# Kernel tuning notes

Measured on AMD Instinct MI355X. Metric: run time of the kernel, lower is better.

Reference implementation:

```python
import jax, jax.numpy as jnp
import numpy as np

NEG_SLOPE = 0.2  # PyG GATConv default negative_slope


def _gat_layer(x, src, dst, n_nodes, W, a_src, a_dst, b):
    # x: [N, din]; src/dst: [E] (self-loops already included)
    h = x @ W                                  # [N, dout]
    s_src = h @ a_src                          # [N]
    s_dst = h @ a_dst                          # [N]
    e = jax.nn.leaky_relu(s_src[src] + s_dst[dst], NEG_SLOPE)  # [E]
    # per-target-node softmax over incoming edges (stable via segment max)
    m = jax.ops.segment_max(e, dst, num_segments=n_nodes)      # [N]
    a = jnp.exp(e - m[dst])                    # [E]
    denom = jax.ops.segment_sum(a, dst, num_segments=n_nodes)  # [N]
    msg = h[src] * a[:, None]                  # [E, dout]
    agg = jax.ops.segment_sum(msg, dst, num_segments=n_nodes)  # [N, dout]
    return agg / denom[:, None] + b


def setup_inputs() -> dict:
    key = jax.random.key(0)
    ks = jax.random.split(key, 16)
    N, E = 100000, 1600000
    in_dim, hid_dim, out_dim = 128, 128, 64
    x = jax.random.normal(ks[0], (N, in_dim), dtype=jnp.float32)
    edge_idx = jax.random.randint(ks[1], (2, E), 0, N, dtype=jnp.int32)

    def lin(k, din, dout):
        return jax.random.normal(k, (din, dout), dtype=jnp.float32) * (1.0 / np.sqrt(din))

    def att(k, dout):
        return jax.random.normal(k, (dout,), dtype=jnp.float32) * (1.0 / np.sqrt(dout))

    return {
        "x": x, "edge_idx": edge_idx,
        "W1": lin(ks[2], in_dim, hid_dim), "as1": att(ks[3], hid_dim), "ad1": att(ks[4], hid_dim), "b1": jnp.zeros((hid_dim,), jnp.float32),
        "W2": lin(ks[5], hid_dim, hid_dim), "as2": att(ks[6], hid_dim), "ad2": att(ks[7], hid_dim), "b2": jnp.zeros((hid_dim,), jnp.float32),
        "W3": lin(ks[8], hid_dim, out_dim), "as3": att(ks[9], out_dim), "ad3": att(ks[10], out_dim), "b3": jnp.zeros((out_dim,), jnp.float32),
    }


def reference(x, edge_idx, W1, as1, ad1, b1, W2, as2, ad2, b2, W3, as3, ad3, b3):
    N = x.shape[0]
    # add self-loops (PyG GATConv default add_self_loops=True)
    loops = jnp.arange(N, dtype=edge_idx.dtype)
    src = jnp.concatenate([edge_idx[0], loops])
    dst = jnp.concatenate([edge_idx[1], loops])
    h = _gat_layer(x, src, dst, N, W1, as1, ad1, b1)
    h = _gat_layer(h, src, dst, N, W2, as2, ad2, b2)
    h = _gat_layer(h, src, dst, N, W3, as3, ad3, b3)
    return jnp.mean(h, axis=-2)  # [out_dim]
```

## Files before the change

### kernel.cpp

```cpp
#include <hip/hip_runtime.h>

static inline int ceil_div(long long a, long long b) { return (int)((a + b - 1) / b); }

typedef __attribute__((ext_vector_type(8))) short bf16x8;
typedef __attribute__((ext_vector_type(4))) float f32x4;

#define TILE 8192
#define BKSH 9

__device__ __forceinline__ float lrelu(float t) { return t > 0.f ? t : 0.2f * t; }

__device__ __forceinline__ void atomAddF(float* p, float v) {
  unsafeAtomicAdd(p, v);
}

__device__ __forceinline__ unsigned int f2bf(float f) {
  unsigned int u = __float_as_uint(f);
  unsigned int r = ((u >> 16) & 1u) + 0x7fffu;
  return (u + r) >> 16;
}

__global__ void cvt_bf16(const float* __restrict__ X, unsigned short* __restrict__ Xb, int n4) {
  int i = blockIdx.x * blockDim.x + threadIdx.x;
  if (i < n4) {
    const float4 v = ((const float4*)X)[i];
    uint2 o;
    o.x = f2bf(v.x) | (f2bf(v.y) << 16);
    o.y = f2bf(v.z) | (f2bf(v.w) << 16);
    ((uint2*)Xb)[i] = o;
  }
}

__global__ void transpose_all(const float* __restrict__ W1, const float* __restrict__ W2,
                              const float* __restrict__ W3, unsigned short* __restrict__ Wt1,
                              unsigned short* __restrict__ Wt2, unsigned short* __restrict__ Wt3) {
  int idx = blockIdx.x * blockDim.x + threadIdx.x;
  const float* W; unsigned short* Wt; int local, DOUTv;
  if (idx < 16384)      { W = W1; Wt = Wt1; local = idx;          DOUTv = 128; }
  else if (idx < 32768) { W = W2; Wt = Wt2; local = idx - 16384;  DOUTv = 128; }
  else if (idx < 40960) { W = W3; Wt = Wt3; local = idx - 32768;  DOUTv = 64;  }
  else return;
  const int k = local / DOUTv, n = local % DOUTv;
  Wt[n * 128 + k] = (unsigned short)f2bf(W[local]);
}

template<int DOUT>
__launch_bounds__(256)
__global__ void gemm_mfma(const unsigned short* __restrict__ Xb, const unsigned short* __restrict__ Wt,
                          const float* __restrict__ avs, const float* __restrict__ avd,
                          unsigned short* __restrict__ Hb, float* __restrict__ Ss,
                          float* __restrict__ Sd, int N, int RG) {
  constexpr int DIN = 128;
  constexpr int CG = DOUT / 64;
  constexpr int RPB = 4 / CG;
  __shared__ float sps[RPB][2][64], spd[RPB][2][64];

  const int wv = threadIdx.x >> 6;
  const int rgl = wv / CG;
  const int cg  = wv % CG;
  const int rg = blockIdx.x * RPB + rgl;
  const bool active = rg < RG;
  const int lane = threadIdx.x & 63;
  const int l16 = lane & 15, quad = lane >> 4;
  const int row0 = rg * 64, colw0 = cg * 64;

  if (active) {
    int xoff[4], woff[4];
#pragma unroll
    for (int t = 0; t < 4; t++) {
      int m = row0 + t * 16 + l16; if (m > N - 1) m = N - 1;
      xoff[t] = m * DIN + quad * 8;
      woff[t] = (colw0 + t * 16 + l16) * DIN + quad * 8;
    }

    f32x4 acc[4][4];
#pragma unroll
    for (int a = 0; a < 4; a++)
#pragma unroll
      for (int c = 0; c < 4; c++) acc[a][c] = (f32x4)0.f;

#pragma unroll
    for (int kk = 0; kk < 4; kk++) {
      bf16x8 aw[4], bx[4];
#pragma unroll
      for (int t = 0; t < 4; t++) aw[t] = *(const bf16x8*)(Wt + woff[t] + kk * 32);
#pragma unroll
      for (int t = 0; t < 4; t++) bx[t] = *(const bf16x8*)(Xb + xoff[t] + kk * 32);
#pragma unroll
      for (int wt = 0; wt < 4; wt++)
#pragma unroll
        for (int xt = 0; xt < 4; xt++)
          acc[wt][xt] = __builtin_amdgcn_mfma_f32_16x16x32_bf16(aw[wt], bx[xt], acc[wt][xt], 0, 0, 0);
    }

    float4 af[4], df[4];
#pragma unroll
    for (int wt = 0; wt < 4; wt++) {
      af[wt] = *(const float4*)(avs + colw0 + wt * 16 + quad * 4);
      df[wt] = *(const float4*)(avd + colw0 + wt * 16 + quad * 4);
    }
#pragma unroll
    for (int xt = 0; xt < 4; xt++) {
      const int m = row0 + xt * 16 + l16;
      float ps = 0.f, pd = 0.f;
#pragma unroll
      for (int wt = 0; wt < 4; wt++) {
        const f32x4 c = acc[wt][xt];
        ps += c[0]*af[wt].x + c[1]*af[wt].y + c[2]*af[wt].z + c[3]*af[wt].w;
        pd += c[0]*df[wt].x + c[1]*df[wt].y + c[2]*df[wt].z + c[3]*df[wt].w;
      }
      ps += __shfl_xor(ps, 16); ps += __shfl_xor(ps, 32);
      pd += __shfl_xor(pd, 16); pd += __shfl_xor(pd, 32);
      if (quad == 0) {
        if (CG == 2) {
          sps[rgl][cg][xt * 16 + l16] = ps;
          spd[rgl][cg][xt * 16 + l16] = pd;
        } else if (m < N) {
          Ss[m] = ps; Sd[m] = pd;
        }
      }
      if (m < N) {
        unsigned short* hp = Hb + (size_t)m * DOUT + colw0 + quad * 4;
#pragma unroll
        for (int wt = 0; wt < 4; wt++) {
          const f32x4 c = acc[wt][xt];
          uint2 o;
          o.x = f2bf(c[0]) | (f2bf(c[1]) << 16);
          o.y = f2bf(c[2]) | (f2bf(c[3]) << 16);
          *(uint2*)(hp + wt * 16) = o;
        }
      }
    }
  }
  if (CG == 2) {
    __syncthreads();
    if (active && cg == 0) {
      const int m = row0 + lane;
      if (m < N) {
        Ss[m] = sps[rgl][0][lane] + sps[rgl][1][lane];
        Sd[m] = spd[rgl][0][lane] + spd[rgl][1][lane];
      }
    }
  }
}

__launch_bounds__(256)
__global__ void bucket_hist(const int* __restrict__ dstv, int* __restrict__ bh,
                            int E, int NBUK) {
  __shared__ int h[256];
  h[threadIdx.x] = 0;
  __syncthreads();
  const int base = blockIdx.x * TILE;
  const int end = min(E, base + TILE);
  for (int i = base + threadIdx.x; i < end; i += 256)
    atomicAdd(&h[dstv[i] >> BKSH], 1);
  __syncthreads();
  if (threadIdx.x < NBUK) bh[blockIdx.x * NBUK + threadIdx.x] = h[threadIdx.x];
}

__launch_bounds__(256)
__global__ void col_scan(int* __restrict__ bh, int* __restrict__ tot, int NBA, int NBUK) {
  __shared__ int sc[256];
  const int t = threadIdx.x;
  const int b = blockIdx.x;
  int carry = 0;
  for (int c0 = 0; c0 < NBA; c0 += 256) {
    const int idx = c0 + t;
    const int v = (idx < NBA) ? bh[idx * NBUK + b] : 0;
    sc[t] = v;
    __syncthreads();
    for (int off = 1; off < 256; off <<= 1) {
      int u = (t >= off) ? sc[t - off] : 0;
      __syncthreads();
      sc[t] += u;
      __syncthreads();
    }
    if (idx < NBA) bh[idx * NBUK + b] = carry + sc[t] - v;
    carry += sc[255];
    __syncthreads();
  }
  if (t == 0) tot[b] = carry;
}

__launch_bounds__(256)
__global__ void base_scan(const int* __restrict__ tot, int* __restrict__ bucketBase,
                          int* __restrict__ rowptr_N, int NBUK, int E) {
  __shared__ int sc[256];
  const int t = threadIdx.x;
  int carry = 0;
  for (int c0 = 0; c0 < NBUK; c0 += 256) {
    const int idx = c0 + t;
    const int v = (idx < NBUK) ? tot[idx] : 0;
    sc[t] = v;
    __syncthreads();
    for (int off = 1; off < 256; off <<= 1) {
      int u = (t >= off) ? sc[t - off] : 0;
      __syncthreads();
      sc[t] += u;
      __syncthreads();
    }
    if (idx < NBUK) bucketBase[idx] = carry + sc[t] - v;
    carry += sc[255];
    __syncthreads();
  }
  if (t == 0) { bucketBase[NBUK] = E; *rowptr_N = E; }
}

__launch_bounds__(256)
__global__ void bucket_scatter(const int* __restrict__ src, const int* __restrict__ dstv,
                               const int* __restrict__ bh, const int* __restrict__ bucketBase,
                               unsigned int* __restrict__ pairs, int E, int NBUK) {
  __shared__ int ofs[256];
  if (threadIdx.x < NBUK)
    ofs[threadIdx.x] = bh[blockIdx.x * NBUK + threadIdx.x] + bucketBase[threadIdx.x];
  __syncthreads();
  const int base = blockIdx.x * TILE;
  const int end = min(E, base + TILE);
  for (int i = base + threadIdx.x; i < end; i += 256) {
    const int d = dstv[i];
    const int pos = atomicAdd(&ofs[d >> BKSH], 1);
    pairs[pos] = ((unsigned int)src[i] << BKSH) | (unsigned int)(d & ((1 << BKSH) - 1));
  }
}

__launch_bounds__(256)
__global__ void region_build(const unsigned int* __restrict__ pairs,
                             const int* __restrict__ bucketBase,
                             int* __restrict__ rowptr, int* __restrict__ srcs, int N) {
  __shared__ int cnt[512], ofs[512], ps[256];
  const int t = threadIdx.x;
  const int r = blockIdx.x;
  const int p0 = bucketBase[r], p1 = bucketBase[r + 1];
  cnt[t] = 0; cnt[t + 256] = 0;
  __syncthreads();
  for (int i = p0 + t; i < p1; i += 256)
    atomicAdd(&cnt[pairs[i] & 511u], 1);
  __syncthreads();
  const int c0 = cnt[2 * t], c1 = cnt[2 * t + 1];
  const int pr = c0 + c1;
  ps[t] = pr;
  __syncthreads();
  for (int off = 1; off < 256; off <<= 1) {
    int v = (t >= off) ? ps[t - off] : 0;
    __syncthreads();
    ps[t] += v;
    __syncthreads();
  }
  const int pbase = ps[t] - pr;
  ofs[2 * t] = pbase; ofs[2 * t + 1] = pbase + c0;
  __syncthreads();
  {
    const int d0 = (r << BKSH) + t;
    if (d0 < N) rowptr[d0] = p0 + ofs[t];
    const int d1 = (r << BKSH) + t + 256;
    if (d1 < N) rowptr[d1] = p0 + ofs[t + 256];
  }
  __syncthreads();
  for (int i = p0 + t; i < p1; i += 256) {
    const unsigned int w = pairs[i];
    const int pos = atomicAdd(&ofs[w & 511u], 1);
    srcs[p0 + pos] = (int)(w >> BKSH);
  }
}

template<int DOUT, bool OBF>
__launch_bounds__(256)
__global__ void node_gather(const int* __restrict__ rowptr, const int* __restrict__ srcs,
                            const float* __restrict__ Ss, const float* __restrict__ Sd,
                            const unsigned short* __restrict__ Hb, const float* __restrict__ b,
                            float* __restrict__ out, unsigned short* __restrict__ outb, int N) {
  constexpr int EPL = DOUT / 16;
  __shared__ uint2 swL[16][18];

  const int l16 = threadIdx.x & 15;
  const int grp = threadIdx.x >> 4;
  const int node = blockIdx.x * 16 + grp;
  if (node >= N) return;

  const int r0 = rowptr[node], r1 = rowptr[node + 1];
  const int deg = r1 - r0;
  const float sd = Sd[node];
  const float wself = __expf(lrelu(Ss[node] + sd));

  float acc[EPL];
#pragma unroll
  for (int k = 0; k < EPL; k++) acc[k] = 0.f;
  float lsum = 0.f;
  const size_t colb = (size_t)l16 * EPL;

  for (int j0 = 0; j0 < deg; j0 += 16) {
    const int idx = j0 + l16;
    int s = node; float w = 0.f;
    if (idx < deg) {
      s = srcs[r0 + idx];
      w = __expf(lrelu(Ss[s] + sd));
    }
    lsum += w;
    swL[grp][l16] = make_uint2((unsigned)s, __float_as_uint(w));
    const int cnt = min(16, deg - j0);
    int t = 0;
    for (; t + 4 <= cnt; t += 4) {
      const uint2 sw0 = swL[grp][t],     sw1 = swL[grp][t + 1];
      const uint2 sw2 = swL[grp][t + 2], sw3 = swL[grp][t + 3];
      const float w0 = __uint_as_float(sw0.y), w1 = __uint_as_float(sw1.y);
      const float w2 = __uint_as_float(sw2.y), w3 = __uint_as_float(sw3.y);
      if (EPL == 8) {
        const uint4 u0 = *(const uint4*)(Hb + (size_t)sw0.x * DOUT + colb);
        const uint4 u1 = *(const uint4*)(Hb + (size_t)sw1.x * DOUT + colb);
        const uint4 u2 = *(const uint4*)(Hb + (size_t)sw2.x * DOUT + colb);
        const uint4 u3 = *(const uint4*)(Hb + (size_t)sw3.x * DOUT + colb);
        const unsigned int a0[4] = {u0.x,u0.y,u0.z,u0.w}, a1[4] = {u1.x,u1.y,u1.z,u1.w};
        const unsigned int a2[4] = {u2.x,u2.y,u2.z,u2.w}, a3[4] = {u3.x,u3.y,u3.z,u3.w};
#pragma unroll
        for (int k = 0; k < 4; k++) {
          acc[2*k]   += __uint_as_float(a0[k] << 16) * w0 + __uint_as_float(a1[k] << 16) * w1
                      + __uint_as_float(a2[k] << 16) * w2 + __uint_as_float(a3[k] << 16) * w3;
          acc[2*k+1] += __uint_as_float(a0[k] & 0xffff0000u) * w0 + __uint_as_float(a1[k] & 0xffff0000u) * w1
                      + __uint_as_float(a2[k] & 0xffff0000u) * w2 + __uint_as_float(a3[k] & 0xffff0000u) * w3;
        }
      } else {
        const uint2 u0 = *(const uint2*)(Hb + (size_t)sw0.x * DOUT + colb);
        const uint2 u1 = *(const uint2*)(Hb + (size_t)sw1.x * DOUT + colb);
        const uint2 u2 = *(const uint2*)(Hb + (size_t)sw2.x * DOUT + colb);
        const uint2 u3 = *(const uint2*)(Hb + (size_t)sw3.x * DOUT + colb);
        const unsigned int a0[2] = {u0.x,u0.y}, a1[2] = {u1.x,u1.y};
        const unsigned int a2[2] = {u2.x,u2.y}, a3[2] = {u3.x,u3.y};
#pragma unroll
        for (int k = 0; k < 2; k++) {
          acc[2*k]   += __uint_as_float(a0[k] << 16) * w0 + __uint_as_float(a1[k] << 16) * w1
                      + __uint_as_float(a2[k] << 16) * w2 + __uint_as_float(a3[k] << 16) * w3;
          acc[2*k+1] += __uint_as_float(a0[k] & 0xffff0000u) * w0 + __uint_as_float(a1[k] & 0xffff0000u) * w1
                      + __uint_as_float(a2[k] & 0xffff0000u) * w2 + __uint_as_float(a3[k] & 0xffff0000u) * w3;
        }
      }
    }
    for (; t < cnt; t++) {
      const uint2 sw = swL[grp][t];
      const float w0 = __uint_as_float(sw.y);
      const unsigned short* pp = Hb + (size_t)sw.x * DOUT + colb;
#pragma unroll
      for (int k = 0; k < EPL / 2; k++) {
        const unsigned int u = ((const unsigned int*)pp)[k];
        acc[2*k]   += __uint_as_float(u << 16) * w0;
        acc[2*k+1] += __uint_as_float(u & 0xffff0000u) * w0;
      }
    }
  }

#pragma unroll
  for (int off = 8; off; off >>= 1) lsum += __shfl_xor(lsum, off);

  {
    const unsigned short* pp = Hb + (size_t)node * DOUT + colb;
#pragma unroll
    for (int k = 0; k < EPL / 2; k++) {
      const unsigned int u = ((const unsigned int*)pp)[k];
      acc[2*k]   += __uint_as_float(u << 16) * wself;
      acc[2*k+1] += __uint_as_float(u & 0xffff0000u) * wself;
    }
  }
  const float inv = 1.f / (lsum + wself);

  float o[EPL];
#pragma unroll
  for (int k = 0; k < EPL; k++) o[k] = acc[k] * inv + b[colb + k];
  if (OBF) {
    if (EPL == 8) {
      uint4 u;
      u.x = f2bf(o[0]) | (f2bf(o[1]) << 16);
      u.y = f2bf(o[2]) | (f2bf(o[3]) << 16);
      u.z = f2bf(o[4]) | (f2bf(o[5]) << 16);
      u.w = f2bf(o[6]) | (f2bf(o[7]) << 16);
      *(uint4*)(outb + (size_t)node * DOUT + colb) = u;
    } else {
      uint2 u;
      u.x = f2bf(o[0]) | (f2bf(o[1]) << 16);
      u.y = f2bf(o[2]) | (f2bf(o[3]) << 16);
      *(uint2*)(outb + (size_t)node * DOUT + colb) = u;
    }
  } else {
    float* op = out + (size_t)node * DOUT + colb;
#pragma unroll
    for (int k = 0; k < EPL; k += 4)
      *(float4*)(op + k) = make_float4(o[k], o[k+1], o[k+2], o[k+3]);
  }
}

__global__ void mean64(const float* __restrict__ Hf, float* __restrict__ out, int N, float scale) {
  __shared__ float sm[256];
  const int col = threadIdx.x & 63;
  const int seg = threadIdx.x >> 6;
  const int stride = gridDim.x * 4;
  float s = 0.f;
  for (int n = blockIdx.x * 4 + seg; n < N; n += stride) s += Hf[(size_t)n * 64 + col];
  sm[threadIdx.x] = s;
  __syncthreads();
  if (seg == 0) {
    float tot = sm[col] + sm[64 + col] + sm[128 + col] + sm[192 + col];
    atomAddF(&out[col], tot * scale);
  }
}

extern "C" void kernel_launch(void* const* d_in, const int* in_sizes, int n_in,
                              void* d_out, int out_size, void* d_ws, size_t ws_size,
                              hipStream_t stream) {
  const float* x   = (const float*)d_in[0];
  const int*   ei  = (const int*)d_in[1];
  const float* W1  = (const float*)d_in[2];
  const float* as1 = (const float*)d_in[3];
  const float* ad1 = (const float*)d_in[4];
  const float* b1  = (const float*)d_in[5];
  const float* W2  = (const float*)d_in[6];
  const float* as2 = (const float*)d_in[7];
  const float* ad2 = (const float*)d_in[8];
  const float* b2  = (const float*)d_in[9];
  const float* W3  = (const float*)d_in[10];
  const float* as3 = (const float*)d_in[11];
  const float* ad3 = (const float*)d_in[12];
  const float* b3  = (const float*)d_in[13];

  const int N = in_sizes[0] / 128;
  const int E = in_sizes[1] / 2;
  const int* src  = ei;
  const int* dstv = ei + E;
  const int RG = ceil_div(N, 64);
  const int NBA = ceil_div(E, TILE);
  const int NBUK = ceil_div(N, 1 << BKSH);

  float* p = (float*)d_ws;
  float* bufA = p; p += (size_t)N * 64;
  float* SsSd = p; p += (size_t)2 * N;
  float* Ss = SsSd, *Sd = SsSd + N;
  unsigned short* Xb = (unsigned short*)p; p += (size_t)N * 64;
  unsigned short* Hb = (unsigned short*)p; p += (size_t)N * 64;
  unsigned short* Wt1 = (unsigned short*)p; p += 128 * 128 / 2;
  unsigned short* Wt2 = (unsigned short*)p; p += 128 * 128 / 2;
  unsigned short* Wt3 = (unsigned short*)p; p += 128 * 64 / 2;
  int* ip = (int*)p;
  int* rowptr     = ip; ip += N + 1;
  int* bh         = ip; ip += (size_t)NBA * NBUK;
  int* tot        = ip; ip += NBUK;
  int* bucketBase = ip; ip += NBUK + 1;
  unsigned int* pairs = (unsigned int*)ip; ip += E;
  int* srcs       = ip; ip += E;

  bucket_hist<<<NBA, 256, 0, stream>>>(dstv, bh, E, NBUK);
  col_scan<<<NBUK, 256, 0, stream>>>(bh, tot, NBA, NBUK);
  base_scan<<<1, 256, 0, stream>>>(tot, bucketBase, rowptr + N, NBUK, E);
  bucket_scatter<<<NBA, 256, 0, stream>>>(src, dstv, bh, bucketBase, pairs, E, NBUK);
  region_build<<<NBUK, 256, 0, stream>>>(pairs, bucketBase, rowptr, srcs, N);

  transpose_all<<<ceil_div(40960, 256), 256, 0, stream>>>(W1, W2, W3, Wt1, Wt2, Wt3);
  cvt_bf16<<<ceil_div((long long)N * 32, 256), 256, 0, stream>>>(x, Xb, N * 32);

  const int GG = ceil_div(N, 16);
  gemm_mfma<128><<<ceil_div(RG, 2), 256, 0, stream>>>(Xb, Wt1, as1, ad1, Hb, Ss, Sd, N, RG);
  node_gather<128, true><<<GG, 256, 0, stream>>>(rowptr, srcs, Ss, Sd, Hb, b1, nullptr, Xb, N);
  gemm_mfma<128><<<ceil_div(RG, 2), 256, 0, stream>>>(Xb, Wt2, as2, ad2, Hb, Ss, Sd, N, RG);
  node_gather<128, true><<<GG, 256, 0, stream>>>(rowptr, srcs, Ss, Sd, Hb, b2, nullptr, Xb, N);
  gemm_mfma<64><<<ceil_div(RG, 4), 256, 0, stream>>>(Xb, Wt3, as3, ad3, Hb, Ss, Sd, N, RG);
  node_gather<64, false><<<GG, 256, 0, stream>>>(rowptr, srcs, Ss, Sd, Hb, b3, bufA, nullptr, N);

  hipMemsetAsync(d_out, 0, 64 * sizeof(float), stream);
  mean64<<<256, 256, 0, stream>>>(bufA, (float*)d_out, N, 1.0f / (float)N);
}
```

Before: 437.7 us.

## Fuse CSR build into cooperative kernel, merge prep kernels, fold mean into gather

The five CSR-construction kernels are merged into one cooperative kernel that separates its phases with grid-wide syncs. The bf16 conversion of x and the weight transposes now run in a single launch. The final layer's gather accumulates the column mean directly through shared and global atomics, which removes the fp32 intermediate buffer and the separate mean kernel. This cuts launch count and an N×64 write/read, at the cost of a CSR build capped at 256 blocks and many global atomics on the 64 outputs.

```diff
diff --git a/kernel.cpp b/kernel.cpp
--- a/kernel.cpp
+++ b/kernel.cpp
@@ -1,4 +1,5 @@
 #include <hip/hip_runtime.h>
+#include <hip/hip_cooperative_groups.h>
 
 static inline int ceil_div(long long a, long long b) { return (int)((a + b - 1) / b); }
 
@@ -20,7 +21,10 @@
   return (u + r) >> 16;
 }
 
-__global__ void cvt_bf16(const float* __restrict__ X, unsigned short* __restrict__ Xb, int n4) {
+__global__ void prep_all(const float* __restrict__ X, unsigned short* __restrict__ Xb, int n4,
+                         const float* __restrict__ W1, const float* __restrict__ W2,
+                         const float* __restrict__ W3, unsigned short* __restrict__ Wt1,
+                         unsigned short* __restrict__ Wt2, unsigned short* __restrict__ Wt3) {
   int i = blockIdx.x * blockDim.x + threadIdx.x;
   if (i < n4) {
     const float4 v = ((const float4*)X)[i];
@@ -28,20 +32,16 @@
     o.x = f2bf(v.x) | (f2bf(v.y) << 16);
     o.y = f2bf(v.z) | (f2bf(v.w) << 16);
     ((uint2*)Xb)[i] = o;
-  }
-}
-
-__global__ void transpose_all(const float* __restrict__ W1, const float* __restrict__ W2,
-                              const float* __restrict__ W3, unsigned short* __restrict__ Wt1,
-                              unsigned short* __restrict__ Wt2, unsigned short* __restrict__ Wt3) {
-  int idx = blockIdx.x * blockDim.x + threadIdx.x;
-  const float* W; unsigned short* Wt; int local, DOUTv;
-  if (idx < 16384)      { W = W1; Wt = Wt1; local = idx;          DOUTv = 128; }
-  else if (idx < 32768) { W = W2; Wt = Wt2; local = idx - 16384;  DOUTv = 128; }
-  else if (idx < 40960) { W = W3; Wt = Wt3; local = idx - 32768;  DOUTv = 64;  }
+    return;
+  }
+  int idx = i - n4;
+  const float* W; unsigned short* Wt; int DOUTv;
+  if (idx < 16384)      { W = W1; Wt = Wt1;               DOUTv = 128; }
+  else if (idx < 32768) { W = W2; Wt = Wt2; idx -= 16384; DOUTv = 128; }
+  else if (idx < 40960) { W = W3; Wt = Wt3; idx -= 32768; DOUTv = 64;  }
   else return;
-  const int k = local / DOUTv, n = local % DOUTv;
-  Wt[n * 128 + k] = (unsigned short)f2bf(W[local]);
+  const int k = idx / DOUTv, n = idx % DOUTv;
+  Wt[n * 128 + k] = (unsigned short)f2bf(W[idx]);
 }
 
 template<int DOUT>
@@ -145,259 +145,237 @@
 }
 
 __launch_bounds__(256)
-__global__ void bucket_hist(const int* __restrict__ dstv, int* __restrict__ bh,
-                            int E, int NBUK) {
-  __shared__ int h[256];
-  h[threadIdx.x] = 0;
-  __syncthreads();
-  const int base = blockIdx.x * TILE;
-  const int end = min(E, base + TILE);
-  for (int i = base + threadIdx.x; i < end; i += 256)
-    atomicAdd(&h[dstv[i] >> BKSH], 1);
-  __syncthreads();
-  if (threadIdx.x < NBUK) bh[blockIdx.x * NBUK + threadIdx.x] = h[threadIdx.x];
-}
-
-__launch_bounds__(256)
-__global__ void col_scan(int* __restrict__ bh, int* __restrict__ tot, int NBA, int NBUK) {
-  __shared__ int sc[256];
+__global__ void coop_csr(const int* __restrict__ src, const int* __restrict__ dstv,
+                         int* __restrict__ bh, int* __restrict__ tot,
+                         int* __restrict__ bucketBase, int* __restrict__ rowptr,
+                         unsigned int* __restrict__ pairs, int* __restrict__ srcs,
+                         int E, int N, int NBA, int NBUK) {
+  namespace cg = cooperative_groups;
+  cg::grid_group grid = cg::this_grid();
+  __shared__ int A[512], Bf[512], Cf[256];
   const int t = threadIdx.x;
-  const int b = blockIdx.x;
-  int carry = 0;
-  for (int c0 = 0; c0 < NBA; c0 += 256) {
-    const int idx = c0 + t;
-    const int v = (idx < NBA) ? bh[idx * NBUK + b] : 0;
-    sc[t] = v;
-    __syncthreads();
+
+  for (int blk = blockIdx.x; blk < NBA; blk += gridDim.x) {
+    A[t] = 0; __syncthreads();
+    const int base = blk * TILE, end = min(E, base + TILE);
+    for (int i = base + t; i < end; i += 256) atomicAdd(&A[dstv[i] >> BKSH], 1);
+    __syncthreads();
+    if (t < NBUK) bh[blk * NBUK + t] = A[t];
+    __syncthreads();
+  }
+  grid.sync();
+
+  for (int b = blockIdx.x; b < NBUK; b += gridDim.x) {
+    int carry = 0;
+    for (int c0 = 0; c0 < NBA; c0 += 256) {
+      const int idx = c0 + t;
+      const int v = (idx < NBA) ? bh[idx * NBUK + b] : 0;
+      A[t] = v; __syncthreads();
+      for (int off = 1; off < 256; off <<= 1) {
+        int u = (t >= off) ? A[t - off] : 0; __syncthreads();
+        A[t] += u; __syncthreads();
+      }
+      if (idx < NBA) bh[idx * NBUK + b] = carry + A[t] - v;
+      carry += A[255]; __syncthreads();
+    }
+    if (t == 0) tot[b] = carry;
+    __syncthreads();
+  }
+  grid.sync();
+
+  if (blockIdx.x == 0) {
+    int carry = 0;
+    for (int c0 = 0; c0 < NBUK; c0 += 256) {
+      const int idx = c0 + t;
+      const int v = (idx < NBUK) ? tot[idx] : 0;
+      A[t] = v; __syncthreads();
+      for (int off = 1; off < 256; off <<= 1) {
+        int u = (t >= off) ? A[t - off] : 0; __syncthreads();
+        A[t] += u; __syncthreads();
+      }
+      if (idx < NBUK) bucketBase[idx] = carry + A[t] - v;
+      carry += A[255]; __syncthreads();
+    }
+    if (t == 0) { bucketBase[NBUK] = E; rowptr[N] = E; }
+  }
+  grid.sync();
+
+  for (int blk = blockIdx.x; blk < NBA; blk += gridDim.x) {
+    if (t < NBUK) A[t] = bh[blk * NBUK + t] + bucketBase[t];
+    __syncthreads();
+    const int base = blk * TILE, end = min(E, base + TILE);
+    for (int i = base + t; i < end; i += 256) {
+      const int d = dstv[i];
+      const int pos = atomicAdd(&A[d >> BKSH], 1);
+      pairs[pos] = ((unsigned int)src[i] << BKSH) | (unsigned int)(d & ((1 << BKSH) - 1));
+    }
+    __syncthreads();
+  }
+  grid.sync();
+
+  for (int r = blockIdx.x; r < NBUK; r += gridDim.x) {
+    const int p0 = bucketBase[r], p1 = bucketBase[r + 1];
+    A[t] = 0; A[t + 256] = 0; __syncthreads();
+    for (int i = p0 + t; i < p1; i += 256) atomicAdd(&A[pairs[i] & 511u], 1);
+    __syncthreads();
+    const int c0 = A[2 * t], c1 = A[2 * t + 1];
+    const int pr = c0 + c1;
+    Cf[t] = pr; __syncthreads();
     for (int off = 1; off < 256; off <<= 1) {
-      int u = (t >= off) ? sc[t - off] : 0;
-      __syncthreads();
-      sc[t] += u;
-      __syncthreads();
-    }
-    if (idx < NBA) bh[idx * NBUK + b] = carry + sc[t] - v;
-    carry += sc[255];
-    __syncthreads();
-  }
-  if (t == 0) tot[b] = carry;
-}
-
-__launch_bounds__(256)
-__global__ void base_scan(const int* __restrict__ tot, int* __restrict__ bucketBase,
-                          int* __restrict__ rowptr_N, int NBUK, int E) {
-  __shared__ int sc[256];
-  const int t = threadIdx.x;
-  int carry = 0;
-  for (int c0 = 0; c0 < NBUK; c0 += 256) {
-    const int idx = c0 + t;
-    const int v = (idx < NBUK) ? tot[idx] : 0;
-    sc[t] = v;
-    __syncthreads();
-    for (int off = 1; off < 256; off <<= 1) {
-      int u = (t >= off) ? sc[t - off] : 0;
-      __syncthreads();
-      sc[t] += u;
-      __syncthreads();
-    }
-    if (idx < NBUK) bucketBase[idx] = carry + sc[t] - v;
-    carry += sc[255];
-    __syncthreads();
-  }
-  if (t == 0) { bucketBase[NBUK] = E; *rowptr_N = E; }
-}
-
-__launch_bounds__(256)
-__global__ void bucket_scatter(const int* __restrict__ src, const int* __restrict__ dstv,
-                               const int* __restrict__ bh, const int* __restrict__ bucketBase,
-                               unsigned int* __restrict__ pairs, int E, int NBUK) {
-  __shared__ int ofs[256];
-  if (threadIdx.x < NBUK)
-    ofs[threadIdx.x] = bh[blockIdx.x * NBUK + threadIdx.x] + bucketBase[threadIdx.x];
-  __syncthreads();
-  const int base = blockIdx.x * TILE;
-  const int end = min(E, base + TILE);
-  for (int i = base + threadIdx.x; i < end; i += 256) {
-    const int d = dstv[i];
-    const int pos = atomicAdd(&ofs[d >> BKSH], 1);
-    pairs[pos] = ((unsigned int)src[i] << BKSH) | (unsigned int)(d & ((1 << BKSH) - 1));
-  }
-}
-
-__launch_bounds__(256)
-__global__ void region_build(const unsigned int* __restrict__ pairs,
-                             const int* __restrict__ bucketBase,
-                             int* __restrict__ rowptr, int* __restrict__ srcs, int N) {
-  __shared__ int cnt[512], ofs[512], ps[256];
-  const int t = threadIdx.x;
-  const int r = blockIdx.x;
-  const int p0 = bucketBase[r], p1 = bucketBase[r + 1];
-  cnt[t] = 0; cnt[t + 256] = 0;
-  __syncthreads();
-  for (int i = p0 + t; i < p1; i += 256)
-    atomicAdd(&cnt[pairs[i] & 511u], 1);
-  __syncthreads();
-  const int c0 = cnt[2 * t], c1 = cnt[2 * t + 1];
-  const int pr = c0 + c1;
-  ps[t] = pr;
-  __syncthreads();
-  for (int off = 1; off < 256; off <<= 1) {
-    int v = (t >= off) ? ps[t - off] : 0;
-    __syncthreads();
-    ps[t] += v;
-    __syncthreads();
-  }
-  const int pbase = ps[t] - pr;
-  ofs[2 * t] = pbase; ofs[2 * t + 1] = pbase + c0;
-  __syncthreads();
-  {
+      int v = (t >= off) ? Cf[t - off] : 0; __syncthreads();
+      Cf[t] += v; __syncthreads();
+    }
+    const int pbase = Cf[t] - pr;
+    Bf[2 * t] = pbase; Bf[2 * t + 1] = pbase + c0;
+    __syncthreads();
     const int d0 = (r << BKSH) + t;
-    if (d0 < N) rowptr[d0] = p0 + ofs[t];
-    const int d1 = (r << BKSH) + t + 256;
-    if (d1 < N) rowptr[d1] = p0 + ofs[t + 256];
-  }
-  __syncthreads();
-  for (int i = p0 + t; i < p1; i += 256) {
-    const unsigned int w = pairs[i];
-    const int pos = atomicAdd(&ofs[w & 511u], 1);
-    srcs[p0 + pos] = (int)(w >> BKSH);
-  }
-}
-
-template<int DOUT, bool OBF>
+    if (d0 < N) rowptr[d0] = p0 + Bf[t];
+    const int d1 = d0 + 256;
+    if (d1 < N) rowptr[d1] = p0 + Bf[t + 256];
+    __syncthreads();
+    for (int i = p0 + t; i < p1; i += 256) {
+      const unsigned int w = pairs[i];
+      const int pos = atomicAdd(&Bf[w & 511u], 1);
+      srcs[p0 + pos] = (int)(w >> BKSH);
+    }
+    __syncthreads();
+  }
+}
+
+template<int DOUT, bool OBF, bool MEAN>
 __launch_bounds__(256)
 __global__ void node_gather(const int* __restrict__ rowptr, const int* __restrict__ srcs,
                             const float* __restrict__ Ss, const float* __restrict__ Sd,
                             const unsigned short* __restrict__ Hb, const float* __restrict__ b,
-                            float* __restrict__ out, unsigned short* __restrict__ outb, int N) {
+                            unsigned short* __restrict__ outb, float* __restrict__ outMean,
+                            float scale, int N) {
   constexpr int EPL = DOUT / 16;
   __shared__ uint2 swL[16][18];
+  __shared__ float colsum[64];
 
   const int l16 = threadIdx.x & 15;
   const int grp = threadIdx.x >> 4;
   const int node = blockIdx.x * 16 + grp;
-  if (node >= N) return;
-
-  const int r0 = rowptr[node], r1 = rowptr[node + 1];
-  const int deg = r1 - r0;
-  const float sd = Sd[node];
-  const float wself = __expf(lrelu(Ss[node] + sd));
-
-  float acc[EPL];
-#pragma unroll
-  for (int k = 0; k < EPL; k++) acc[k] = 0.f;
-  float lsum = 0.f;
+  if (MEAN) {
+    if (threadIdx.x < 64) colsum[threadIdx.x] = 0.f;
+    __syncthreads();
+  }
+  const bool act = node < N;
   const size_t colb = (size_t)l16 * EPL;
-
-  for (int j0 = 0; j0 < deg; j0 += 16) {
-    const int idx = j0 + l16;
-    int s = node; float w = 0.f;
-    if (idx < deg) {
-      s = srcs[r0 + idx];
-      w = __expf(lrelu(Ss[s] + sd));
-    }
-    lsum += w;
-    swL[grp][l16] = make_uint2((unsigned)s, __float_as_uint(w));
-    const int cnt = min(16, deg - j0);
-    int t = 0;
-    for (; t + 4 <= cnt; t += 4) {
-      const uint2 sw0 = swL[grp][t],     sw1 = swL[grp][t + 1];
-      const uint2 sw2 = swL[grp][t + 2], sw3 = swL[grp][t + 3];
-      const float w0 = __uint_as_float(sw0.y), w1 = __uint_as_float(sw1.y);
-      const float w2 = __uint_as_float(sw2.y), w3 = __uint_as_float(sw3.y);
-      if (EPL == 8) {
-        const uint4 u0 = *(const uint4*)(Hb + (size_t)sw0.x * DOUT + colb);
-        const uint4 u1 = *(const uint4*)(Hb + (size_t)sw1.x * DOUT + colb);
-        const uint4 u2 = *(const uint4*)(Hb + (size_t)sw2.x * DOUT + colb);
-        const uint4 u3 = *(const uint4*)(Hb + (size_t)sw3.x * DOUT + colb);
-        const unsigned int a0[4] = {u0.x,u0.y,u0.z,u0.w}, a1[4] = {u1.x,u1.y,u1.z,u1.w};
-        const unsigned int a2[4] = {u2.x,u2.y,u2.z,u2.w}, a3[4] = {u3.x,u3.y,u3.z,u3.w};
-#pragma unroll
-        for (int k = 0; k < 4; k++) {
-          acc[2*k]   += __uint_as_float(a0[k] << 16) * w0 + __uint_as_float(a1[k] << 16) * w1
-                      + __uint_as_float(a2[k] << 16) * w2 + __uint_as_float(a3[k] << 16) * w3;
-          acc[2*k+1] += __uint_as_float(a0[k] & 0xffff0000u) * w0 + __uint_as_float(a1[k] & 0xffff0000u) * w1
-                      + __uint_as_float(a2[k] & 0xffff0000u) * w2 + __uint_as_float(a3[k] & 0xffff0000u) * w3;
+  float o[EPL];
+#pragma unroll
+  for (int k = 0; k < EPL; k++) o[k] = 0.f;
+
+  if (act) {
+    const int r0 = rowptr[node], r1 = rowptr[node + 1];
+    const int deg = r1 - r0;
+    const float sd = Sd[node];
+    const float wself = __expf(lrelu(Ss[node] + sd));
+
+    float acc[EPL];
+#pragma unroll
+    for (int k = 0; k < EPL; k++) acc[k] = 0.f;
+    float lsum = 0.f;
+
+    for (int j0 = 0; j0 < deg; j0 += 16) {
+      const int idx = j0 + l16;
+      int s = node; float w = 0.f;
+      if (idx < deg) {
+        s = srcs[r0 + idx];
+        w = __expf(lrelu(Ss[s] + sd));
+      }
+      lsum += w;
+      swL[grp][l16] = make_uint2((unsigned)s, __float_as_uint(w));
+      const int cnt = min(16, deg - j0);
+      int t = 0;
+      for (; t + 4 <= cnt; t += 4) {
+        const uint2 sw0 = swL[grp][t],     sw1 = swL[grp][t + 1];
+        const uint2 sw2 = swL[grp][t + 2], sw3 = swL[grp][t + 3];
+        const float w0 = __uint_as_float(sw0.y), w1 = __uint_as_float(sw1.y);
+        const float w2 = __uint_as_float(sw2.y), w3 = __uint_as_float(sw3.y);
+        if (EPL == 8) {
+          const uint4 u0 = *(const uint4*)(Hb + (size_t)sw0.x * DOUT + colb);
+          const uint4 u1 = *(const uint4*)(Hb + (size_t)sw1.x * DOUT + colb);
+          const uint4 u2 = *(const uint4*)(Hb + (size_t)sw2.x * DOUT + colb);
+          const uint4 u3 = *(const uint4*)(Hb + (size_t)sw3.x * DOUT + colb);
+          const unsigned int a0[4] = {u0.x,u0.y,u0.z,u0.w}, a1[4] = {u1.x,u1.y,u1.z,u1.w};
+          const unsigned int a2[4] = {u2.x,u2.y,u2.z,u2.w}, a3[4] = {u3.x,u3.y,u3.z,u3.w};
+#pragma unroll
+          for (int k = 0; k < 4; k++) {
+            acc[2*k]   += __uint_as_float(a0[k] << 16) * w0 + __uint_as_float(a1[k] << 16) * w1
+                        + __uint_as_float(a2[k] << 16) * w2 + __uint_as_float(a3[k] << 16) * w3;
+            acc[2*k+1] += __uint_as_float(a0[k] & 0xffff0000u) * w0 + __uint_as_float(a1[k] & 0xffff0000u) * w1
+                        + __uint_as_float(a2[k] & 0xffff0000u) * w2 + __uint_as_float(a3[k] & 0xffff0000u) * w3;
+          }
+        } else {
+          const uint2 u0 = *(const uint2*)(Hb + (size_t)sw0.x * DOUT + colb);
+          const uint2 u1 = *(const uint2*)(Hb + (size_t)sw1.x * DOUT + colb);
+          const uint2 u2 = *(const uint2*)(Hb + (size_t)sw2.x * DOUT + colb);
+          const uint2 u3 = *(const uint2*)(Hb + (size_t)sw3.x * DOUT + colb);
+          const unsigned int a0[2] = {u0.x,u0.y}, a1[2] = {u1.x,u1.y};
+          const unsigned int a2[2] = {u2.x,u2.y}, a3[2] = {u3.x,u3.y};
+#pragma unroll
+          for (int k = 0; k < 2; k++) {
+            acc[2*k]   += __uint_as_float(a0[k] << 16) * w0 + __uint_as_float(a1[k] << 16) * w1
+                        + __uint_as_float(a2[k] << 16) * w2 + __uint_as_float(a3[k] << 16) * w3;
+            acc[2*k+1] += __uint_as_float(a0[k] & 0xffff0000u) * w0 + __uint_as_float(a1[k] & 0xffff0000u) * w1
+                        + __uint_as_float(a2[k] & 0xffff0000u) * w2 + __uint_as_float(a3[k] & 0xffff0000u) * w3;
+          }
         }
-      } else {
-        const uint2 u0 = *(const uint2*)(Hb + (size_t)sw0.x * DOUT + colb);
-        const uint2 u1 = *(const uint2*)(Hb + (size_t)sw1.x * DOUT + colb);
-        const uint2 u2 = *(const uint2*)(Hb + (size_t)sw2.x * DOUT + colb);
-        const uint2 u3 = *(const uint2*)(Hb + (size_t)sw3.x * DOUT + colb);
-        const unsigned int a0[2] = {u0.x,u0.y}, a1[2] = {u1.x,u1.y};
-        const unsigned int a2[2] = {u2.x,u2.y}, a3[2] = {u3.x,u3.y};
-#pragma unroll
-        for (int k = 0; k < 2; k++) {
-          acc[2*k]   += __uint_as_float(a0[k] << 16) * w0 + __uint_as_float(a1[k] << 16) * w1
-                      + __uint_as_float(a2[k] << 16) * w2 + __uint_as_float(a3[k] << 16) * w3;
-          acc[2*k+1] += __uint_as_float(a0[k] & 0xffff0000u) * w0 + __uint_as_float(a1[k] & 0xffff0000u) * w1
-                      + __uint_as_float(a2[k] & 0xffff0000u) * w2 + __uint_as_float(a3[k] & 0xffff0000u) * w3;
+      }
+      for (; t < cnt; t++) {
+        const uint2 sw = swL[grp][t];
+        const float w0 = __uint_as_float(sw.y);
+        const unsigned short* pp = Hb + (size_t)sw.x * DOUT + colb;
+#pragma unroll
+        for (int k = 0; k < EPL / 2; k++) {
+          const unsigned int u = ((const unsigned int*)pp)[k];
+          acc[2*k]   += __uint_as_float(u << 16) * w0;
+          acc[2*k+1] += __uint_as_float(u & 0xffff0000u) * w0;
         }
       }
     }
-    for (; t < cnt; t++) {
-      const uint2 sw = swL[grp][t];
-      const float w0 = __uint_as_float(sw.y);
-      const unsigned short* pp = Hb + (size_t)sw.x * DOUT + colb;
+
+#pragma unroll
+    for (int off = 8; off; off >>= 1) lsum += __shfl_xor(lsum, off);
+
+    {
+      const unsigned short* pp = Hb + (size_t)node * DOUT + colb;
 #pragma unroll
       for (int k = 0; k < EPL / 2; k++) {
         const unsigned int u = ((const unsigned int*)pp)[k];
-        acc[2*k]   += __uint_as_float(u << 16) * w0;
-        acc[2*k+1] += __uint_as_float(u & 0xffff0000u) * w0;
-      }
-    }
-  }
-
-#pragma unroll
-  for (int off = 8; off; off >>= 1) lsum += __shfl_xor(lsum, off);
-
-  {
-    const unsigned short* pp = Hb + (size_t)node * DOUT + colb;
-#pragma unroll
-    for (int k = 0; k < EPL / 2; k++) {
-      const unsigned int u = ((const unsigned int*)pp)[k];
-      acc[2*k]   += __uint_as_float(u << 16) * wself;
-      acc[2*k+1] += __uint_as_float(u & 0xffff0000u) * wself;
-    }
-  }
-  const float inv = 1.f / (lsum + wself);
-
-  float o[EPL];
-#pragma unroll
-  for (int k = 0; k < EPL; k++) o[k] = acc[k] * inv + b[colb + k];
-  if (OBF) {
-    if (EPL == 8) {
-      uint4 u;
-      u.x = f2bf(o[0]) | (f2bf(o[1]) << 16);
-      u.y = f2bf(o[2]) | (f2bf(o[3]) << 16);
-      u.z = f2bf(o[4]) | (f2bf(o[5]) << 16);
-      u.w = f2bf(o[6]) | (f2bf(o[7]) << 16);
-      *(uint4*)(outb + (size_t)node * DOUT + colb) = u;
-    } else {
-      uint2 u;
-      u.x = f2bf(o[0]) | (f2bf(o[1]) << 16);
-      u.y = f2bf(o[2]) | (f2bf(o[3]) << 16);
-      *(uint2*)(outb + (size_t)node * DOUT + colb) = u;
-    }
-  } else {
-    float* op = out + (size_t)node * DOUT + colb;
-#pragma unroll
-    for (int k = 0; k < EPL; k += 4)
-      *(float4*)(op + k) = make_float4(o[k], o[k+1], o[k+2], o[k+3]);
-  }
-}
-
-__global__ void mean64(const float* __restrict__ Hf, float* __restrict__ out, int N, float scale) {
-  __shared__ float sm[256];
-  const int col = threadIdx.x & 63;
-  const int seg = threadIdx.x >> 6;
-  const int stride = gridDim.x * 4;
-  float s = 0.f;
-  for (int n = blockIdx.x * 4 + seg; n < N; n += stride) s += Hf[(size_t)n * 64 + col];
-  sm[threadIdx.x] = s;
-  __syncthreads();
-  if (seg == 0) {
-    float tot = sm[col] + sm[64 + col] + sm[128 + col] + sm[192 + col];
-    atomAddF(&out[col], tot * scale);
+        acc[2*k]   += __uint_as_float(u << 16) * wself;
+        acc[2*k+1] += __uint_as_float(u & 0xffff0000u) * wself;
+      }
+    }
+    const float inv = 1.f / (lsum + wself);
+#pragma unroll
+    for (int k = 0; k < EPL; k++) o[k] = acc[k] * inv + b[colb + k];
+
+    if (OBF) {
+      if (EPL == 8) {
+        uint4 u;
+        u.x = f2bf(o[0]) | (f2bf(o[1]) << 16);
+        u.y = f2bf(o[2]) | (f2bf(o[3]) << 16);
+        u.z = f2bf(o[4]) | (f2bf(o[5]) << 16);
+        u.w = f2bf(o[6]) | (f2bf(o[7]) << 16);
+        *(uint4*)(outb + (size_t)node * DOUT + colb) = u;
+      } else {
+        uint2 u;
+        u.x = f2bf(o[0]) | (f2bf(o[1]) << 16);
+        u.y = f2bf(o[2]) | (f2bf(o[3]) << 16);
+        *(uint2*)(outb + (size_t)node * DOUT + colb) = u;
+      }
+    }
+  }
+
+  if (MEAN) {
+    if (act) {
+#pragma unroll
+      for (int k = 0; k < EPL; k++) atomicAdd(&colsum[colb + k], o[k]);
+    }
+    __syncthreads();
+    if (threadIdx.x < 64) atomAddF(&outMean[threadIdx.x], colsum[threadIdx.x] * scale);
   }
 }
 
@@ -428,9 +406,8 @@
   const int NBUK = ceil_div(N, 1 << BKSH);
 
   float* p = (float*)d_ws;
-  float* bufA = p; p += (size_t)N * 64;
   float* SsSd = p; p += (size_t)2 * N;
-  float* Ss = SsSd, *Sd = SsSd + N;
+  float* Ss = SsSd; float* Sd = SsSd + N;
   unsigned short* Xb = (unsigned short*)p; p += (size_t)N * 64;
   unsigned short* Hb = (unsigned short*)p; p += (size_t)N * 64;
   unsigned short* Wt1 = (unsigned short*)p; p += 128 * 128 / 2;
@@ -444,23 +421,27 @@
   unsigned int* pairs = (unsigned int*)ip; ip += E;
   int* srcs       = ip; ip += E;
 
-  bucket_hist<<<NBA, 256, 0, stream>>>(dstv, bh, E, NBUK);
-  col_scan<<<NBUK, 256, 0, stream>>>(bh, tot, NBA, NBUK);
-  base_scan<<<1, 256, 0, stream>>>(tot, bucketBase, rowptr + N, NBUK, E);
-  bucket_scatter<<<NBA, 256, 0, stream>>>(src, dstv, bh, bucketBase, pairs, E, NBUK);
-  region_build<<<NBUK, 256, 0, stream>>>(pairs, bucketBase, rowptr, srcs, N);
-
-  transpose_all<<<ceil_div(40960, 256), 256, 0, stream>>>(W1, W2, W3, Wt1, Wt2, Wt3);
-  cvt_bf16<<<ceil_div((long long)N * 32, 256), 256, 0, stream>>>(x, Xb, N * 32);
+  hipMemsetAsync(d_out, 0, 64 * sizeof(float), stream);
+
+  {
+    int G = (NBA > NBUK) ? NBA : NBUK;
+    if (G > 256) G = 256;
+    void* args[] = {(void*)&src, (void*)&dstv, (void*)&bh, (void*)&tot,
+                    (void*)&bucketBase, (void*)&rowptr, (void*)&pairs, (void*)&srcs,
+                    (void*)&E, (void*)&N, (void*)&NBA, (void*)&NBUK};
+    hipLaunchCooperativeKernel((const void*)coop_csr, dim3(G), dim3(256), args, 0, stream);
+  }
+
+  const int n4 = N * 32;
+  prep_all<<<ceil_div((long long)n4 + 40960, 256), 256, 0, stream>>>(
+      x, Xb, n4, W1, W2, W3, Wt1, Wt2, Wt3);
 
   const int GG = ceil_div(N, 16);
+  const float scl = 1.0f / (float)N;
   gemm_mfma<128><<<ceil_div(RG, 2), 256, 0, stream>>>(Xb, Wt1, as1, ad1, Hb, Ss, Sd, N, RG);
-  node_gather<128, true><<<GG, 256, 0, stream>>>(rowptr, srcs, Ss, Sd, Hb, b1, nullptr, Xb, N);
+  node_gather<128, true, false><<<GG, 256, 0, stream>>>(rowptr, srcs, Ss, Sd, Hb, b1, Xb, nullptr, 0.f, N);
   gemm_mfma<128><<<ceil_div(RG, 2), 256, 0, stream>>>(Xb, Wt2, as2, ad2, Hb, Ss, Sd, N, RG);
-  node_gather<128, true><<<GG, 256, 0, stream>>>(rowptr, srcs, Ss, Sd, Hb, b2, nullptr, Xb, N);
+  node_gather<128, true, false><<<GG, 256, 0, stream>>>(rowptr, srcs, Ss, Sd, Hb, b2, Xb, nullptr, 0.f, N);
   gemm_mfma<64><<<ceil_div(RG, 4), 256, 0, stream>>>(Xb, Wt3, as3, ad3, Hb, Ss, Sd, N, RG);
-  node_gather<64, false><<<GG, 256, 0, stream>>>(rowptr, srcs, Ss, Sd, Hb, b3, bufA, nullptr, N);
-
-  hipMemsetAsync(d_out, 0, 64 * sizeof(float), stream);
-  mean64<<<256, 256, 0, stream>>>(bufA, (float*)d_out, N, 1.0f / (float)N);
-}
+  node_gather<64, false, true><<<GG, 256, 0, stream>>>(rowptr, srcs, Ss, Sd, Hb, b3, nullptr, (float*)d_out, scl, N);
+}
```

After: 647.6 us. 48.0% more time.
